# Kernel optimization log

Measured on AMD Instinct MI355X. Metric: run time of the kernel, lower is better.

## Reference

```python
import jax, jax.numpy as jnp
import numpy as np
import math

B, S, D, H = 2, 2048, 1024, 16
DH = D // H          # 64 head dim
BLK = 64             # SpargeAttn block size
TOPK = 0.5           # fraction of KV blocks kept per query block
NEG = -1e9


def setup_inputs() -> dict:
    key = jax.random.key(0)
    ks = jax.random.split(key, 8)
    s = 0.02
    return {
        "inputs": jax.random.normal(ks[0], (B, S, D), dtype=jnp.float32),
        "ln_g": jnp.ones((D,), jnp.float32),
        "ln_b": jnp.zeros((D,), jnp.float32),
        "Wq": jax.random.normal(ks[1], (D, D), jnp.float32) * s,
        "bq": jnp.zeros((D,), jnp.float32),
        "Wk": jax.random.normal(ks[2], (D, D), jnp.float32) * s,
        "bk": jnp.zeros((D,), jnp.float32),
        "Wv": jax.random.normal(ks[3], (D, D), jnp.float32) * s,
        "bv": jnp.zeros((D,), jnp.float32),
        "Wo": jax.random.normal(ks[4], (D, D), jnp.float32) * s,
        "bo": jnp.zeros((D,), jnp.float32),
    }


def _sparse_topk_attn(q, k, v):
    # q,k,v: [B,H,S,DH]. Block-mean-similarity top-k sparse causal attention
    # (SpargeAttn spas_sage2_attn_meansim_topk, fp32 reference semantics).
    nb = S // BLK
    qm = q.reshape(B, H, nb, BLK, DH).mean(3)          # [B,H,nb,DH]
    km = k.reshape(B, H, nb, BLK, DH).mean(3)
    sim = jnp.einsum('bhqd,bhkd->bhqk', qm, km)        # block similarity
    cblk = jnp.tril(jnp.ones((nb, nb), bool))          # causal block mask
    sim = jnp.where(cblk, sim, NEG)
    kk = max(1, int(math.ceil(TOPK * nb)))
    _, idx = jax.lax.top_k(sim, kk)                    # [B,H,nb,kk]
    blk = jax.nn.one_hot(idx, nb, dtype=jnp.float32).sum(-2) > 0  # [B,H,nb,nb]
    blk = (blk & cblk) | jnp.eye(nb, dtype=bool)       # keep diagonal block
    tok_mask = jnp.repeat(jnp.repeat(blk, BLK, axis=2), BLK, axis=3)  # [B,H,S,S]
    tok_mask = tok_mask & jnp.tril(jnp.ones((S, S), bool))
    scores = jnp.einsum('bhid,bhjd->bhij', q, k) / jnp.float32(math.sqrt(DH))
    scores = jnp.where(tok_mask, scores, NEG)
    p = jax.nn.softmax(scores, axis=-1)
    return jnp.einsum('bhij,bhjd->bhid', p, v)


def reference(inputs, ln_g, ln_b, Wq, bq, Wk, bk, Wv, bv, Wo, bo):
    # pre-norm LayerNorm
    mu = inputs.mean(-1, keepdims=True)
    var = inputs.var(-1, keepdims=True)
    x = (inputs - mu) * jax.lax.rsqrt(var + 1e-5) * ln_g + ln_b
    # QKV projections -> [B,H,S,DH]
    q = (x @ Wq + bq).reshape(B, S, H, DH).transpose(0, 2, 1, 3)
    k = (x @ Wk + bk).reshape(B, S, H, DH).transpose(0, 2, 1, 3)
    v = (x @ Wv + bv).reshape(B, S, H, DH).transpose(0, 2, 1, 3)
    ctx = _sparse_topk_attn(q, k, v)
    ctx = ctx.transpose(0, 2, 1, 3).reshape(B, S, D)
    return ctx @ Wo + bo
```

## Files before the change

### kernel.cpp

```cpp
#include <hip/hip_runtime.h>
#include <stdint.h>

#define DEV static __device__ __forceinline__

typedef __attribute__((ext_vector_type(8))) short s16x8;
typedef __attribute__((ext_vector_type(4))) float f32x4;

constexpr int Bdim = 2, Sdim = 2048, Ddim = 1024, Hdim = 16, DH = 64;
constexpr int Mrows = Bdim * Sdim;
constexpr int NB = 32;
constexpr int SEL_STRIDE = 18;

constexpr size_t OFF_XB    = 0;
constexpr size_t OFF_WTQKV = OFF_XB    + (size_t)Mrows*Ddim*2;
constexpr size_t OFF_WOT   = OFF_WTQKV + (size_t)3072*1024*2;
constexpr size_t OFF_QKV   = OFF_WOT   + (size_t)1024*1024*2;
constexpr size_t OFF_CTX   = OFF_QKV   + (size_t)Mrows*3072*2;
constexpr size_t OFF_XM    = OFF_CTX   + (size_t)Mrows*Ddim*2;
constexpr size_t OFF_QM    = OFF_XM    + (size_t)64*1024*4;
constexpr size_t OFF_KM    = OFF_QM    + (size_t)64*1024*4;
constexpr size_t OFF_BIASQ = OFF_KM    + (size_t)64*1024*4;
constexpr size_t OFF_SEL   = OFF_BIASQ + (size_t)3072*4;
constexpr size_t OFF_PART  = OFF_SEL   + (size_t)1024*SEL_STRIDE*4;

DEV float bf2f(unsigned short u){ union{unsigned int i; float f;} x; x.i = ((unsigned int)u)<<16; return x.f; }
DEV unsigned short f2bf(float f){ union{float f; unsigned int i;} x; x.f=f;
  unsigned int r = x.i + 0x7fffu + ((x.i>>16)&1u); return (unsigned short)(r>>16); }

DEV void gload16(const unsigned short* g, unsigned short* l){
  __builtin_amdgcn_global_load_lds(
      (__attribute__((address_space(1))) void*)(void*)g,
      (__attribute__((address_space(3))) void*)l, 16, 0, 0);
}

DEV unsigned int cvtpk(float a, float b){
  unsigned int r;
  asm("v_cvt_pk_bf16_f32 %0, %1, %2" : "=v"(r) : "v"(a), "v"(b));
  return r;
}

__global__ __launch_bounds__(256) void ln_kernel(const float* __restrict__ inp,
                                                 const float* __restrict__ gam,
                                                 const float* __restrict__ bet,
                                                 unsigned short* __restrict__ xb){
  const int row = blockIdx.x, t = threadIdx.x;
  __shared__ float red[8];
  const float4 v = ((const float4*)(inp + (size_t)row*Ddim))[t];
  float s  = v.x + v.y + v.z + v.w;
  float s2 = v.x*v.x + v.y*v.y + v.z*v.z + v.w*v.w;
#pragma unroll
  for (int mk=32; mk>=1; mk>>=1){ s += __shfl_xor(s, mk); s2 += __shfl_xor(s2, mk); }
  if ((t&63)==0){ red[t>>6] = s; red[4+(t>>6)] = s2; }
  __syncthreads();
  s  = red[0]+red[1]+red[2]+red[3];
  s2 = red[4]+red[5]+red[6]+red[7];
  const float mu  = s * (1.f/Ddim);
  const float var = s2 * (1.f/Ddim) - mu*mu;
  const float rs  = rsqrtf(var + 1e-5f);
  const float4 gv = ((const float4*)gam)[t];
  const float4 bv = ((const float4*)bet)[t];
  float o0 = (v.x-mu)*rs*gv.x + bv.x;
  float o1 = (v.y-mu)*rs*gv.y + bv.y;
  float o2 = (v.z-mu)*rs*gv.z + bv.z;
  float o3 = (v.w-mu)*rs*gv.w + bv.w;
  uint2 u;
  u.x = (unsigned int)f2bf(o0) | ((unsigned int)f2bf(o1)<<16);
  u.y = (unsigned int)f2bf(o2) | ((unsigned int)f2bf(o3)<<16);
  ((uint2*)(xb + (size_t)row*Ddim))[t] = u;
}

__global__ __launch_bounds__(256) void xm_kernel(const float* __restrict__ inp,
                                                 const float* __restrict__ gam,
                                                 const float* __restrict__ bet,
                                                 float* __restrict__ xm){
  const int blk = blockIdx.x, t = threadIdx.x;
  const int w = t>>6, lane = t&63;
  __shared__ float part[4][1024];
  float4 gv[4], bv[4];
#pragma unroll
  for (int p=0;p<4;++p){ gv[p] = ((const float4*)gam)[lane + 64*p];
                         bv[p] = ((const float4*)bet)[lane + 64*p]; }
  float ax[4][4];
#pragma unroll
  for (int p=0;p<4;++p)
#pragma unroll
    for (int c=0;c<4;++c) ax[p][c]=0.f;
  for (int rr=0; rr<16; ++rr){
    const int row = blk*64 + w*16 + rr;
    const float4* rp = (const float4*)(inp + (size_t)row*Ddim);
    float4 v[4]; float s=0.f, s2=0.f;
#pragma unroll
    for (int p=0;p<4;++p){
      v[p] = rp[lane + 64*p];
      s  += v[p].x+v[p].y+v[p].z+v[p].w;
      s2 += v[p].x*v[p].x+v[p].y*v[p].y+v[p].z*v[p].z+v[p].w*v[p].w;
    }
#pragma unroll
    for (int mk=32; mk>=1; mk>>=1){ s += __shfl_xor(s,mk); s2 += __shfl_xor(s2,mk); }
    const float mu = s*(1.f/Ddim);
    const float var = s2*(1.f/Ddim) - mu*mu;
    const float rs = rsqrtf(var + 1e-5f);
#pragma unroll
    for (int p=0;p<4;++p){
      ax[p][0] += (v[p].x-mu)*rs*gv[p].x + bv[p].x;
      ax[p][1] += (v[p].y-mu)*rs*gv[p].y + bv[p].y;
      ax[p][2] += (v[p].z-mu)*rs*gv[p].z + bv[p].z;
      ax[p][3] += (v[p].w-mu)*rs*gv[p].w + bv[p].w;
    }
  }
#pragma unroll
  for (int p=0;p<4;++p){
    float4 o; o.x=ax[p][0]; o.y=ax[p][1]; o.z=ax[p][2]; o.w=ax[p][3];
    ((float4*)&part[w][0])[lane + 64*p] = o;
  }
  __syncthreads();
  float4 r0 = ((float4*)&part[0][0])[t];
  float4 r1 = ((float4*)&part[1][0])[t];
  float4 r2 = ((float4*)&part[2][0])[t];
  float4 r3 = ((float4*)&part[3][0])[t];
  float4 o;
  o.x = (r0.x+r1.x+r2.x+r3.x)*(1.f/64);
  o.y = (r0.y+r1.y+r2.y+r3.y)*(1.f/64);
  o.z = (r0.z+r1.z+r2.z+r3.z)*(1.f/64);
  o.w = (r0.w+r1.w+r2.w+r3.w)*(1.f/64);
  ((float4*)(xm + (size_t)blk*Ddim))[t] = o;
}

__global__ __launch_bounds__(256) void wtrans4_kernel(const float* __restrict__ Wq,
                                                      const float* __restrict__ Wk,
                                                      const float* __restrict__ Wv,
                                                      const float* __restrict__ Wo,
                                                      unsigned short* __restrict__ wtqkv,
                                                      unsigned short* __restrict__ wot){
  __shared__ float tile[32][33];
  const int z = blockIdx.z;
  const float* W = (z==0)?Wq:(z==1)?Wk:(z==2)?Wv:Wo;
  unsigned short* Wt = (z<3) ? (wtqkv + (size_t)z*1024*1024) : wot;
  const int n0 = blockIdx.x*32, k0 = blockIdx.y*32;
  const int t = threadIdx.x, r = t>>5, c = t&31;
#pragma unroll
  for (int i=0;i<4;++i) tile[r+8*i][c] = W[(size_t)(k0 + r + 8*i)*1024 + n0 + c];
  __syncthreads();
#pragma unroll
  for (int i=0;i<4;++i) Wt[(size_t)(n0 + r + 8*i)*1024 + k0 + c] = f2bf(tile[c][r+8*i]);
}

__global__ void biascat_kernel(const float* __restrict__ bq, const float* __restrict__ bk,
                               const float* __restrict__ bv, float* __restrict__ outb){
  int i = blockIdx.x*256 + threadIdx.x;
  float v = (i<1024) ? bq[i] : (i<2048 ? bk[i-1024] : bv[i-2048]);
  outb[i] = v;
}

__global__ __launch_bounds__(256) void qmkm_part(const float* __restrict__ xm,
    const float* __restrict__ Wq, const float* __restrict__ Wk,
    float* __restrict__ part){
  const int c  = blockIdx.x*256 + threadIdx.x;
  const int rg = blockIdx.y >> 3, ks = blockIdx.y & 7;
  const int z  = blockIdx.z;
  const float* W = z ? Wk : Wq;
  const int r0 = rg*16, k0 = ks*128;
  float acc[16];
#pragma unroll
  for (int r=0;r<16;++r) acc[r]=0.f;
  for (int k=0;k<128;k+=4){
    const float wv0 = W[(size_t)(k0+k  )*1024 + c];
    const float wv1 = W[(size_t)(k0+k+1)*1024 + c];
    const float wv2 = W[(size_t)(k0+k+2)*1024 + c];
    const float wv3 = W[(size_t)(k0+k+3)*1024 + c];
#pragma unroll
    for (int r=0;r<16;++r){
      const float4 xv = *(const float4*)&xm[(size_t)(r0+r)*1024 + k0 + k];
      acc[r] = fmaf(xv.w, wv3, fmaf(xv.z, wv2, fmaf(xv.y, wv1, fmaf(xv.x, wv0, acc[r]))));
    }
  }
  float* dst = part + (((size_t)z*8 + ks)*64 + r0)*1024 + c;
#pragma unroll
  for (int r=0;r<16;++r) dst[(size_t)r*1024] = acc[r];
}

__global__ __launch_bounds__(256) void qmkm_reduce(const float* __restrict__ part,
    const float* __restrict__ bq, const float* __restrict__ bk,
    float* __restrict__ qm, float* __restrict__ km){
  const int idx = blockIdx.x*256 + threadIdx.x;
  const int z = blockIdx.y;
  const int c = idx & 1023, r = idx >> 10;
  const float* p = part + ((size_t)z*8*64*1024) + (size_t)r*1024 + c;
  float s = 0.f;
#pragma unroll
  for (int ks=0; ks<8; ++ks) s += p[(size_t)ks*64*1024];
  s += z ? bk[c] : bq[c];
  (z ? km : qm)[(size_t)r*1024 + c] = s;
}

__global__ __launch_bounds__(256) void topk_kernel(const float* __restrict__ qm,
                                                   const float* __restrict__ km,
                                                   int* __restrict__ sel){
  const int bhq = blockIdx.x;
  const int qb = bhq & 31, h = (bhq>>5) & 15, b = bhq >> 9;
  const int t = threadIdx.x;
  __shared__ float sim[32];
  __shared__ int keep[32];
  const int kb = t>>3, l8 = t&7;
  float acc = 0.f;
  if (kb <= qb){
    const float* qv = qm + (size_t)(b*32 + qb)*1024 + h*64;
    const float* kv = km + (size_t)(b*32 + kb)*1024 + h*64;
#pragma unroll
    for (int d=0; d<8; ++d) acc += qv[l8*8+d] * kv[l8*8+d];
  }
  acc += __shfl_xor(acc,1); acc += __shfl_xor(acc,2); acc += __shfl_xor(acc,4);
  if (l8==0) sim[kb] = (kb<=qb) ? acc : -1e30f;
  __syncthreads();
  if (t < 32){
    int k2 = t; int ok = 0;
    if (k2 <= qb){
      float sv = sim[k2]; int rank = 0;
      for (int j=0;j<=qb;++j){
        float sj = sim[j];
        rank += (sj > sv) || (sj == sv && j < k2);
      }
      ok = (rank < 16) || (k2 == qb);
    }
    keep[t] = ok;
  }
  __syncthreads();
  if (t == 0){
    int* dstp = sel + (size_t)bhq * SEL_STRIDE;
    int c = 0;
    for (int j=0;j<32;++j) if (keep[j]) dstp[1+c++] = j;
    dstp[0] = c;
  }
}

template<int OUT_BF16>
__global__ __launch_bounds__(256) void gemm_bt(const unsigned short* __restrict__ A,
                                               const unsigned short* __restrict__ Bt,
                                               const float* __restrict__ bias,
                                               void* __restrict__ C, int N){
  constexpr int K = 1024;
  __shared__ unsigned short ldsA[128*64];
  __shared__ unsigned short ldsB[128*64];
  const int t = threadIdx.x, lane = t & 63, wid = t >> 6;
  const int wr = wid >> 1, wc = wid & 1;
  const int rl = lane & 15, g = lane >> 4;

  const int nbx = gridDim.x;
  const int nwg = nbx * gridDim.y;
  const int id  = blockIdx.y * nbx + blockIdx.x;
  const int nid = (id & 7) * (nwg >> 3) + (id >> 3);
  const int m0 = (nid / nbx) * 128, n0 = (nid % nbx) * 128;

  const f32x4 ZERO4 = {0.f,0.f,0.f,0.f};
  f32x4 acc[4][4];
#pragma unroll
  for (int i=0;i<4;++i)
#pragma unroll
    for (int j=0;j<4;++j) acc[i][j] = ZERO4;

  const unsigned short* Ap[4]; const unsigned short* Bp[4];
  unsigned short* dA[4]; unsigned short* dB[4];
  const int csrc = (lane & 7) ^ (lane >> 3);
#pragma unroll
  for (int i=0;i<4;++i){
    const int row_i = (wid*4+i)*8 + (lane>>3);
    Ap[i] = A  + (size_t)(m0 + row_i)*K + csrc*8;
    Bp[i] = Bt + (size_t)(n0 + row_i)*K + csrc*8;
    dA[i] = ldsA + (wid*4+i)*512;
    dB[i] = ldsB + (wid*4+i)*512;
  }

  for (int k0=0; k0<K; k0+=64){
    __syncthreads();
#pragma unroll
    for (int i=0;i<4;++i){ gload16(Ap[i] + k0, dA[i]); gload16(Bp[i] + k0, dB[i]); }
    __syncthreads();
#pragma unroll
    for (int kk=0;kk<2;++kk){
      s16x8 af[4], bfr[4];
#pragma unroll
      for (int mi=0;mi<4;++mi){
        int row = wr*64 + mi*16 + rl;
        af[mi] = *(const s16x8*)((char*)ldsA + row*128 + (((kk*4+g) ^ (rl&7))<<4));
      }
#pragma unroll
      for (int ni=0;ni<4;++ni){
        int row = wc*64 + ni*16 + rl;
        bfr[ni] = *(const s16x8*)((char*)ldsB + row*128 + (((kk*4+g) ^ (rl&7))<<4));
      }
#pragma unroll
      for (int mi=0;mi<4;++mi)
#pragma unroll
        for (int ni=0;ni<4;++ni)
          acc[mi][ni] = __builtin_amdgcn_mfma_f32_16x16x32_bf16(af[mi], bfr[ni], acc[mi][ni], 0,0,0);
    }
  }

  const int r4 = g*4;
#pragma unroll
  for (int mi=0;mi<4;++mi){
#pragma unroll
    for (int ni=0;ni<4;++ni){
      int col = n0 + wc*64 + ni*16 + rl;
      float bb = bias[col];
#pragma unroll
      for (int e=0;e<4;++e){
        int row = m0 + wr*64 + mi*16 + r4 + e;
        float v = acc[mi][ni][e] + bb;
        if (OUT_BF16) ((unsigned short*)C)[(size_t)row*N + col] = f2bf(v);
        else          ((float*)C)[(size_t)row*N + col] = v;
      }
    }
  }
}

__global__ __launch_bounds__(256) void attn_kernel(const unsigned short* __restrict__ qkv,
                                                   const int* __restrict__ sel,
                                                   unsigned short* __restrict__ ctx){
  const int id = blockIdx.x;
  const int xcd = id & 7, jj = id >> 3;
  const int bh = xcd + 8*(jj/24);
  const int tau = jj % 24;
  const int h = bh & 15, b = bh >> 4;
  int qbl[2]; int nq;
  if (tau < 8){ qbl[0]=tau; qbl[1]=15-tau; nq=2; }
  else        { qbl[0]=tau+8; qbl[1]=0;    nq=1; }

  const int t = threadIdx.x, wid = t >> 6, lane = t & 63;
  const int rl = lane & 15, g = lane >> 4;
  const int q_local = wid*16 + rl;

  __shared__ unsigned short K_s[2][4096];
  __shared__ unsigned short V_s[2][4096];

  const int jst = t >> 2, cq = t & 3;
  const int r2 = t >> 3, dq = t & 7;
  const unsigned short* kbase = qkv + (size_t)(b*Sdim + jst)*3072 + 1024 + h*DH + cq*16;
  const unsigned short* vbase = qkv + (size_t)(b*Sdim + 2*r2)*3072 + 2048 + h*DH + dq*8;
  const int kwb0 = jst*128 + (((cq*2  ) ^ (jst&7))<<4);
  const int kwb1 = jst*128 + (((cq*2+1) ^ (jst&7))<<4);
  const f32x4 ZERO4 = {0.f,0.f,0.f,0.f};

  const int src0 = (rl + 16*((2*g  ) & 3)) << 2;
  const int src1 = (rl + 16*((2*g+1) & 3)) << 2;
  const bool hsel = (g >> 1);

  for (int iq=0; iq<nq; ++iq){
    const int qb = qbl[iq];
    const int* selrow = sel + (size_t)(((b*Hdim)+h)*NB + qb) * SEL_STRIDE;
    const int ns = selrow[0];

    const int qg0 = b*Sdim + qb*64 + q_local;
    const unsigned short* qbase = qkv + (size_t)qg0*3072 + h*DH;
    s16x8 qa[2];
#pragma unroll
    for (int kk=0; kk<2; ++kk){
      s16x8 raw = *(const s16x8*)(qbase + kk*32 + g*8);
      s16x8 qq;
#pragma unroll
      for (int e=0;e<8;++e) qq[e] = (short)f2bf(bf2f((unsigned short)raw[e]) * 0.125f);
      qa[kk] = qq;
    }

    f32x4 o[4];
    float m_r = -3.0e38f, l_r = 0.f;
#pragma unroll
    for (int f=0; f<4; ++f) o[f] = ZERO4;

    __syncthreads();

    int kb = selrow[1];
    s16x8 kr0, kr1, vr0, vr1;
    {
      const size_t off = (size_t)kb*64*3072;
      kr0 = *(const s16x8*)(kbase + off);
      kr1 = *(const s16x8*)(kbase + off + 8);
      vr0 = *(const s16x8*)(vbase + off);
      vr1 = *(const s16x8*)(vbase + off + 3072);
    }

    for (int it=0; it<ns; ++it){
      const int buf = it & 1;
      unsigned short* Kw = &K_s[buf][0];
      unsigned short* Vw = &V_s[buf][0];
      *(s16x8*)((char*)Kw + kwb0) = kr0;
      *(s16x8*)((char*)Kw + kwb1) = kr1;
#pragma unroll
      for (int e=0;e<8;++e){
        const int d1 = dq*8 + e;
        const int sw = (d1&7) ^ (d1>>3);
        const unsigned int pr = (unsigned int)(unsigned short)vr0[e]
                              | ((unsigned int)(unsigned short)vr1[e] << 16);
        *(unsigned int*)((char*)Vw + d1*128 + ((4*r2) ^ (sw<<4))) = pr;
      }
      const int kbcur = kb;
      if (it+1 < ns){
        kb = selrow[2+it];
        const size_t off = (size_t)kb*64*3072;
        kr0 = *(const s16x8*)(kbase + off);
        kr1 = *(const s16x8*)(kbase + off + 8);
        vr0 = *(const s16x8*)(vbase + off);
        vr1 = *(const s16x8*)(vbase + off + 3072);
      }
      __syncthreads();

      f32x4 sfT[4];
#pragma unroll
      for (int f=0;f<4;++f) sfT[f] = ZERO4;
#pragma unroll
      for (int kk=0;kk<2;++kk){
#pragma unroll
        for (int f=0;f<4;++f){
          const int jr = f*16 + rl;
          s16x8 kf = *(const s16x8*)((char*)Kw + jr*128 + (((kk*4+g) ^ (jr&7))<<4));
          sfT[f] = __builtin_amdgcn_mfma_f32_16x16x32_bf16(kf, qa[kk], sfT[f], 0,0,0);
        }
      }
      if (kbcur == qb){
#pragma unroll
        for (int f=0;f<4;++f)
#pragma unroll
          for (int e=0;e<4;++e){
            const int j = f*16 + g*4 + e;
            if (j > q_local) sfT[f][e] = -1e9f;
          }
      }
      {
        float mx = sfT[0][0];
#pragma unroll
        for (int f=0;f<4;++f)
#pragma unroll
          for (int e=0;e<4;++e) mx = fmaxf(mx, sfT[f][e]);
        mx = fmaxf(mx, __shfl_xor(mx, 16));
        mx = fmaxf(mx, __shfl_xor(mx, 32));
        const float mn = fmaxf(m_r, mx);
        const float al = __expf(m_r - mn);
        m_r = mn;
        float rs = 0.f;
#pragma unroll
        for (int f=0;f<4;++f)
#pragma unroll
          for (int e=0;e<4;++e){
            const float p = __expf(sfT[f][e] - mn);
            sfT[f][e] = p; rs += p;
          }
        rs += __shfl_xor(rs, 16);
        rs += __shfl_xor(rs, 32);
        l_r = l_r*al + rs;
#pragma unroll
        for (int f=0;f<4;++f)
#pragma unroll
          for (int e=0;e<4;++e) o[f][e] *= al;
      }

      unsigned int plo[4], phi[4];
#pragma unroll
      for (int f=0;f<4;++f){
        plo[f] = cvtpk(sfT[f][0], sfT[f][1]);
        phi[f] = cvtpk(sfT[f][2], sfT[f][3]);
      }

#pragma unroll
      for (int kk=0;kk<2;++kk){
        const int f0 = 2*kk, f1 = 2*kk+1;
        unsigned int a0, b0, w0, w1, w2, w3;
        a0 = __builtin_amdgcn_ds_bpermute(src0, plo[f0]);
        b0 = __builtin_amdgcn_ds_bpermute(src0, plo[f1]);
        w0 = hsel ? b0 : a0;
        a0 = __builtin_amdgcn_ds_bpermute(src0, phi[f0]);
        b0 = __builtin_amdgcn_ds_bpermute(src0, phi[f1]);
        w1 = hsel ? b0 : a0;
        a0 = __builtin_amdgcn_ds_bpermute(src1, plo[f0]);
        b0 = __builtin_amdgcn_ds_bpermute(src1, plo[f1]);
        w2 = hsel ? b0 : a0;
        a0 = __builtin_amdgcn_ds_bpermute(src1, phi[f0]);
        b0 = __builtin_amdgcn_ds_bpermute(src1, phi[f1]);
        w3 = hsel ? b0 : a0;
        union { unsigned int u[4]; s16x8 v; } pfc;
        pfc.u[0] = w0; pfc.u[1] = w1; pfc.u[2] = w2; pfc.u[3] = w3;
        const s16x8 pf = pfc.v;
#pragma unroll
        for (int f=0;f<4;++f){
          const int d = f*16 + rl;
          const int sw = (d&7) ^ (d>>3);
          s16x8 vf = *(const s16x8*)((char*)Vw + d*128 + ((64*kk + 16*g) ^ (sw<<4)));
          o[f] = __builtin_amdgcn_mfma_f32_16x16x32_bf16(vf, pf, o[f], 0,0,0);
        }
      }
    }

    {
      const float inv = 1.f / l_r;
      unsigned short* crow = ctx + (size_t)qg0*Ddim + h*DH;
#pragma unroll
      for (int f=0;f<4;++f){
        uint2 st;
        st.x = (unsigned int)f2bf(o[f][0]*inv) | ((unsigned int)f2bf(o[f][1]*inv)<<16);
        st.y = (unsigned int)f2bf(o[f][2]*inv) | ((unsigned int)f2bf(o[f][3]*inv)<<16);
        *(uint2*)(crow + f*16 + g*4) = st;
      }
    }
  }
}

extern "C" void kernel_launch(void* const* d_in, const int* in_sizes, int n_in,
                              void* d_out, int out_size, void* d_ws, size_t ws_size,
                              hipStream_t stream){
  (void)in_sizes; (void)n_in; (void)out_size; (void)ws_size;
  const float* inp  = (const float*)d_in[0];
  const float* ln_g = (const float*)d_in[1];
  const float* ln_b = (const float*)d_in[2];
  const float* Wq   = (const float*)d_in[3];
  const float* bq   = (const float*)d_in[4];
  const float* Wk   = (const float*)d_in[5];
  const float* bk   = (const float*)d_in[6];
  const float* Wv   = (const float*)d_in[7];
  const float* bv   = (const float*)d_in[8];
  const float* Wo   = (const float*)d_in[9];
  const float* bo   = (const float*)d_in[10];

  char* ws = (char*)d_ws;
  unsigned short* xb    = (unsigned short*)(ws + OFF_XB);
  unsigned short* wtqkv = (unsigned short*)(ws + OFF_WTQKV);
  unsigned short* wot   = (unsigned short*)(ws + OFF_WOT);
  unsigned short* qkvb  = (unsigned short*)(ws + OFF_QKV);
  unsigned short* ctx   = (unsigned short*)(ws + OFF_CTX);
  float* xm   = (float*)(ws + OFF_XM);
  float* qm   = (float*)(ws + OFF_QM);
  float* km   = (float*)(ws + OFF_KM);
  float* bqkv = (float*)(ws + OFF_BIASQ);
  int*   sel  = (int*)(ws + OFF_SEL);
  float* part = (float*)(ws + OFF_PART);

  ln_kernel<<<Mrows, 256, 0, stream>>>(inp, ln_g, ln_b, xb);
  xm_kernel<<<64, 256, 0, stream>>>(inp, ln_g, ln_b, xm);
  wtrans4_kernel<<<dim3(32,32,4), 256, 0, stream>>>(Wq, Wk, Wv, Wo, wtqkv, wot);
  biascat_kernel<<<12, 256, 0, stream>>>(bq, bk, bv, bqkv);
  qmkm_part<<<dim3(4,32,2), 256, 0, stream>>>(xm, Wq, Wk, part);
  qmkm_reduce<<<dim3(256,2), 256, 0, stream>>>(part, bq, bk, qm, km);
  topk_kernel<<<1024, 256, 0, stream>>>(qm, km, sel);
  gemm_bt<1><<<dim3(24,32), 256, 0, stream>>>(xb, wtqkv, bqkv, (void*)qkvb, 3072);
  attn_kernel<<<768, 256, 0, stream>>>(qkvb, sel, ctx);
  gemm_bt<0><<<dim3(8,32), 256, 0, stream>>>(ctx, wot, bo, d_out, 1024);
}
```

Baseline: 155.3 us.

## Double-buffer GEMM LDS stages and fold bias concat into weight transpose

```diff
diff --git a/kernel.cpp b/kernel.cpp
--- a/kernel.cpp
+++ b/kernel.cpp
@@ -130,26 +130,28 @@
                                                       const float* __restrict__ Wk,
                                                       const float* __restrict__ Wv,
                                                       const float* __restrict__ Wo,
+                                                      const float* __restrict__ bq,
+                                                      const float* __restrict__ bk,
+                                                      const float* __restrict__ bv,
                                                       unsigned short* __restrict__ wtqkv,
-                                                      unsigned short* __restrict__ wot){
+                                                      unsigned short* __restrict__ wot,
+                                                      float* __restrict__ bqkv){
   __shared__ float tile[32][33];
   const int z = blockIdx.z;
   const float* W = (z==0)?Wq:(z==1)?Wk:(z==2)?Wv:Wo;
   unsigned short* Wt = (z<3) ? (wtqkv + (size_t)z*1024*1024) : wot;
   const int n0 = blockIdx.x*32, k0 = blockIdx.y*32;
   const int t = threadIdx.x, r = t>>5, c = t&31;
+  if (z<3 && blockIdx.x==0 && blockIdx.y==0){
+    const float* bb = (z==0)?bq:(z==1)?bk:bv;
+#pragma unroll
+    for (int i=0;i<4;++i) bqkv[z*1024 + t + 256*i] = bb[t + 256*i];
+  }
 #pragma unroll
   for (int i=0;i<4;++i) tile[r+8*i][c] = W[(size_t)(k0 + r + 8*i)*1024 + n0 + c];
   __syncthreads();
 #pragma unroll
   for (int i=0;i<4;++i) Wt[(size_t)(n0 + r + 8*i)*1024 + k0 + c] = f2bf(tile[c][r+8*i]);
-}
-
-__global__ void biascat_kernel(const float* __restrict__ bq, const float* __restrict__ bk,
-                               const float* __restrict__ bv, float* __restrict__ outb){
-  int i = blockIdx.x*256 + threadIdx.x;
-  float v = (i<1024) ? bq[i] : (i<2048 ? bk[i-1024] : bv[i-2048]);
-  outb[i] = v;
 }
 
 __global__ __launch_bounds__(256) void qmkm_part(const float* __restrict__ xm,
@@ -233,14 +235,40 @@
   }
 }
 
+#define G_STAGE(bsel, kofs) do { \
+  gload16(A0 + (kofs), ldsA + (bsel)*4096 + (wid*2+0)*512); \
+  gload16(A1 + (kofs), ldsA + (bsel)*4096 + (wid*2+1)*512); \
+  gload16(B0 + (kofs), ldsB + (bsel)*4096 + (wid*2+0)*512); \
+  gload16(B1 + (kofs), ldsB + (bsel)*4096 + (wid*2+1)*512); \
+} while(0)
+
+#define G_COMPUTE(bsel) do { \
+  s16x8 af[4], bfr[4]; \
+  _Pragma("unroll") \
+  for (int mi=0;mi<4;++mi){ \
+    int row = wr*64 + mi*16 + rl; \
+    af[mi] = *(const s16x8*)((char*)ldsA + (bsel)*8192 + row*64 + ((g ^ ((row>>1)&3))<<4)); \
+  } \
+  _Pragma("unroll") \
+  for (int ni=0;ni<4;++ni){ \
+    int row = wc*64 + ni*16 + rl; \
+    bfr[ni] = *(const s16x8*)((char*)ldsB + (bsel)*8192 + row*64 + ((g ^ ((row>>1)&3))<<4)); \
+  } \
+  _Pragma("unroll") \
+  for (int mi=0;mi<4;++mi) \
+    _Pragma("unroll") \
+    for (int ni=0;ni<4;++ni) \
+      acc[mi][ni] = __builtin_amdgcn_mfma_f32_16x16x32_bf16(af[mi], bfr[ni], acc[mi][ni], 0,0,0); \
+} while(0)
+
 template<int OUT_BF16>
 __global__ __launch_bounds__(256) void gemm_bt(const unsigned short* __restrict__ A,
                                                const unsigned short* __restrict__ Bt,
                                                const float* __restrict__ bias,
                                                void* __restrict__ C, int N){
   constexpr int K = 1024;
-  __shared__ unsigned short ldsA[128*64];
-  __shared__ unsigned short ldsB[128*64];
+  __shared__ unsigned short ldsA[2*128*32];
+  __shared__ unsigned short ldsB[2*128*32];
   const int t = threadIdx.x, lane = t & 63, wid = t >> 6;
   const int wr = wid >> 1, wc = wid & 1;
   const int rl = lane & 15, g = lane >> 4;
@@ -258,42 +286,24 @@
 #pragma unroll
     for (int j=0;j<4;++j) acc[i][j] = ZERO4;
 
-  const unsigned short* Ap[4]; const unsigned short* Bp[4];
-  unsigned short* dA[4]; unsigned short* dB[4];
-  const int csrc = (lane & 7) ^ (lane >> 3);
-#pragma unroll
-  for (int i=0;i<4;++i){
-    const int row_i = (wid*4+i)*8 + (lane>>3);
-    Ap[i] = A  + (size_t)(m0 + row_i)*K + csrc*8;
-    Bp[i] = Bt + (size_t)(n0 + row_i)*K + csrc*8;
-    dA[i] = ldsA + (wid*4+i)*512;
-    dB[i] = ldsB + (wid*4+i)*512;
-  }
+  const int slot0 = wid*128 + lane, slot1 = slot0 + 64;
+  const int sr0 = slot0>>2, sc0 = slot0&3;
+  const int sr1 = slot1>>2, sc1 = slot1&3;
+  const unsigned short* A0 = A  + (size_t)(m0 + sr0)*K + (sc0 ^ ((sr0>>1)&3))*8;
+  const unsigned short* A1 = A  + (size_t)(m0 + sr1)*K + (sc1 ^ ((sr1>>1)&3))*8;
+  const unsigned short* B0 = Bt + (size_t)(n0 + sr0)*K + (sc0 ^ ((sr0>>1)&3))*8;
+  const unsigned short* B1 = Bt + (size_t)(n0 + sr1)*K + (sc1 ^ ((sr1>>1)&3))*8;
+
+  G_STAGE(0, 0);
+  __syncthreads();
 
   for (int k0=0; k0<K; k0+=64){
+    G_STAGE(1, k0+32);
+    G_COMPUTE(0);
     __syncthreads();
-#pragma unroll
-    for (int i=0;i<4;++i){ gload16(Ap[i] + k0, dA[i]); gload16(Bp[i] + k0, dB[i]); }
+    if (k0+64 < K) G_STAGE(0, k0+64);
+    G_COMPUTE(1);
     __syncthreads();
-#pragma unroll
-    for (int kk=0;kk<2;++kk){
-      s16x8 af[4], bfr[4];
-#pragma unroll
-      for (int mi=0;mi<4;++mi){
-        int row = wr*64 + mi*16 + rl;
-        af[mi] = *(const s16x8*)((char*)ldsA + row*128 + (((kk*4+g) ^ (rl&7))<<4));
-      }
-#pragma unroll
-      for (int ni=0;ni<4;++ni){
-        int row = wc*64 + ni*16 + rl;
-        bfr[ni] = *(const s16x8*)((char*)ldsB + row*128 + (((kk*4+g) ^ (rl&7))<<4));
-      }
-#pragma unroll
-      for (int mi=0;mi<4;++mi)
-#pragma unroll
-        for (int ni=0;ni<4;++ni)
-          acc[mi][ni] = __builtin_amdgcn_mfma_f32_16x16x32_bf16(af[mi], bfr[ni], acc[mi][ni], 0,0,0);
-    }
   }
 
   const int r4 = g*4;
@@ -534,8 +544,7 @@
 
   ln_kernel<<<Mrows, 256, 0, stream>>>(inp, ln_g, ln_b, xb);
   xm_kernel<<<64, 256, 0, stream>>>(inp, ln_g, ln_b, xm);
-  wtrans4_kernel<<<dim3(32,32,4), 256, 0, stream>>>(Wq, Wk, Wv, Wo, wtqkv, wot);
-  biascat_kernel<<<12, 256, 0, stream>>>(bq, bk, bv, bqkv);
+  wtrans4_kernel<<<dim3(32,32,4), 256, 0, stream>>>(Wq, Wk, Wv, Wo, bq, bk, bv, wtqkv, wot, bqkv);
   qmkm_part<<<dim3(4,32,2), 256, 0, stream>>>(xm, Wq, Wk, part);
   qmkm_reduce<<<dim3(256,2), 256, 0, stream>>>(part, bq, bk, qm, km);
   topk_kernel<<<1024, 256, 0, stream>>>(qm, km, sel);
```

Measured after the change: 164.0 us. 5.6% more time.
